# Optimization experiments

Hardware: AMD Instinct MI355X
Metric: run time of the kernel (lower is better)

## Reference

```python
import jax, jax.numpy as jnp
import numpy as np
from jax import lax

B, H, G, T = 16384, 128, 5, 12

def setup_inputs() -> dict:
    key = jax.random.key(0)
    ks = jax.random.split(key, 12)
    s = 0.05  # weight scale for numerical sanity
    return {
        "encoder_hidden": jax.random.normal(ks[0], (B, H), jnp.float32),
        "encoder_cell": jax.random.normal(ks[1], (B, H), jnp.float32),
        "last_position": jax.random.normal(ks[2], (B, 2), jnp.float32),
        "gp_w1": jax.random.normal(ks[3], (H, H), jnp.float32) * s,
        "gp_b1": jnp.zeros((H,), jnp.float32),
        "gp_w2": jax.random.normal(ks[4], (H, G * 2), jnp.float32) * s,
        "gp_b2": jnp.zeros((G * 2,), jnp.float32),
        "pr_w1": jax.random.normal(ks[5], (H, H // 2), jnp.float32) * s,
        "pr_b1": jnp.zeros((H // 2,), jnp.float32),
        "pr_w2": jax.random.normal(ks[6], (H // 2, G), jnp.float32) * s,
        "pr_b2": jnp.zeros((G,), jnp.float32),
        "w_ih": jax.random.normal(ks[7], (4, 4 * H), jnp.float32) * s,   # LSTM input weights [in=4, 4H] (i,f,g,o)
        "w_hh": jax.random.normal(ks[8], (H, 4 * H), jnp.float32) * s,   # LSTM recurrent weights [H, 4H]
        "b_ih": jnp.zeros((4 * H,), jnp.float32),
        "b_hh": jnp.zeros((4 * H,), jnp.float32),
        "ph_w": jax.random.normal(ks[9], (H, 2), jnp.float32) * s,
        "ph_b": jnp.zeros((2,), jnp.float32),
    }

def reference(encoder_hidden, encoder_cell, last_position,
              gp_w1, gp_b1, gp_w2, gp_b2,
              pr_w1, pr_b1, pr_w2, pr_b2,
              w_ih, w_hh, b_ih, b_hh, ph_w, ph_b):
    b = encoder_hidden.shape[0]
    # goal prediction: residual on last_position
    g_hid = jax.nn.relu(encoder_hidden @ gp_w1 + gp_b1)
    goals = (g_hid @ gp_w2 + gp_b2).reshape(b, G, 2) + last_position[:, None, :]  # [B,G,2]
    # goal probabilities
    p_hid = jax.nn.relu(encoder_hidden @ pr_w1 + pr_b1)
    goal_probs = jax.nn.softmax(p_hid @ pr_w2 + pr_b2, axis=-1)  # [B,G]
    # batch all goals together: leading goal dim [G,B,...]
    goals_gb = jnp.swapaxes(goals, 0, 1)                      # [G,B,2]
    h0 = jnp.broadcast_to(encoder_hidden, (G, b, H))
    c0 = jnp.broadcast_to(encoder_cell, (G, b, H))
    pos0 = jnp.broadcast_to(last_position, (G, b, 2))
    bias = b_ih + b_hh

    def step(carry, _):
        pos, h, c = carry
        x = jnp.concatenate([pos, goals_gb], axis=-1)          # [G,B,4]
        gates = x @ w_ih + h @ w_hh + bias                      # [G,B,4H]
        i, f, g, o = jnp.split(gates, 4, axis=-1)
        c_new = jax.nn.sigmoid(f) * c + jax.nn.sigmoid(i) * jnp.tanh(g)
        h_new = jax.nn.sigmoid(o) * jnp.tanh(c_new)
        pos_new = pos + (h_new @ ph_w + ph_b)                   # residual position update
        return (pos_new, h_new, c_new), pos_new

    _, path = lax.scan(step, (pos0, h0, c0), None, length=T)   # [T,G,B,2]
    predictions = jnp.transpose(path, (2, 1, 0, 3))            # [B,G,T,2]
    return predictions, goals, goal_probs
```

## Files before the change

kernel.cpp:

```cpp
#include <hip/hip_runtime.h>

#define Bn 16384
#define Hn 128
#define Gn 5
#define Tn 12

typedef __attribute__((ext_vector_type(8))) __bf16 bf16x8;
typedef __attribute__((ext_vector_type(4))) float f32x4;
typedef __attribute__((ext_vector_type(4))) unsigned int u32x4;
typedef __attribute__((ext_vector_type(2))) unsigned int u32x2;
typedef unsigned int u32;
typedef unsigned short u16;

#define MFMA(a, b, c) __builtin_amdgcn_mfma_f32_16x16x32_bf16((a), (b), (c), 0, 0, 0)

__device__ __forceinline__ u16 f2bf(float f) { return __builtin_bit_cast(u16, (__bf16)f); }
__device__ __forceinline__ u32 pk2(float a, float b) { return (u32)f2bf(a) | ((u32)f2bf(b) << 16); }

__device__ __forceinline__ int hbsw(int row, int bytein) {
    return row * 256 + ((((bytein >> 4) ^ row) & 15) << 4) + (bytein & 15);
}
__device__ __forceinline__ int pbsw(int row, int bytein) {
    return row * 128 + ((((bytein >> 4) ^ row) & 7) << 4) + (bytein & 15);
}

__global__ __launch_bounds__(256) void k_phaseA(
    const float* __restrict__ eh, const float* __restrict__ lastpos,
    const float* __restrict__ gp_w1, const float* __restrict__ gp_b1,
    const float* __restrict__ gp_w2, const float* __restrict__ gp_b2,
    const float* __restrict__ pr_w1, const float* __restrict__ pr_b1,
    const float* __restrict__ pr_w2, const float* __restrict__ pr_b2,
    float* __restrict__ goals_o, float* __restrict__ probs_o)
{
    __shared__ __align__(16) char eT[64 * 256];
    __shared__ __align__(16) char gT[64 * 256];
    __shared__ __align__(16) char pT[64 * 128];
    __shared__ float lgT[64 * 8];

    const int tid = threadIdx.x;
    const int lane = tid & 63;
    const int wv = tid >> 6;
    const int lg = lane >> 4, li = lane & 15;
    const int r0 = blockIdx.x * 64;
    const int rowbase = wv * 16;

    {
        int row = tid >> 2, seg = tid & 3;
        const float* src = eh + (size_t)(r0 + row) * Hn + seg * 32;
#pragma unroll
        for (int cc = 0; cc < 4; ++cc) {
            u32 p0 = pk2(src[cc * 8 + 0], src[cc * 8 + 1]);
            u32 p1 = pk2(src[cc * 8 + 2], src[cc * 8 + 3]);
            u32 p2 = pk2(src[cc * 8 + 4], src[cc * 8 + 5]);
            u32 p3 = pk2(src[cc * 8 + 6], src[cc * 8 + 7]);
            *(u32x4*)(eT + hbsw(row, seg * 64 + cc * 16)) = (u32x4){p0, p1, p2, p3};
        }
    }
    __syncthreads();

    bf16x8 Ae[4];
#pragma unroll
    for (int kc = 0; kc < 4; ++kc)
        Ae[kc] = *(const bf16x8*)(eT + hbsw(rowbase + li, kc * 64 + lg * 16));

#pragma unroll 1
    for (int nt = 0; nt < 8; ++nt) {
        int c1 = nt * 16 + li;
        f32x4 acc = {0.f, 0.f, 0.f, 0.f};
#pragma unroll
        for (int kc = 0; kc < 4; ++kc) {
            bf16x8 bfr;
#pragma unroll
            for (int j = 0; j < 8; ++j)
                bfr[j] = (__bf16)gp_w1[(size_t)(kc * 32 + lg * 8 + j) * Hn + c1];
            acc = MFMA(Ae[kc], bfr, acc);
        }
        float bias = gp_b1[c1];
#pragma unroll
        for (int r = 0; r < 4; ++r) {
            int row = rowbase + lg * 4 + r;
            float v = fmaxf(acc[r] + bias, 0.f);
            *(u16*)(gT + hbsw(row, c1 * 2)) = f2bf(v);
        }
    }
    __syncthreads();

    {
        bf16x8 Ag[4];
#pragma unroll
        for (int kc = 0; kc < 4; ++kc)
            Ag[kc] = *(const bf16x8*)(gT + hbsw(rowbase + li, kc * 64 + lg * 16));
        f32x4 acc = {0.f, 0.f, 0.f, 0.f};
#pragma unroll
        for (int kc = 0; kc < 4; ++kc) {
            bf16x8 bfr;
#pragma unroll
            for (int j = 0; j < 8; ++j) {
                int k = kc * 32 + lg * 8 + j;
                bfr[j] = (li < 10) ? (__bf16)gp_w2[k * 10 + li] : (__bf16)0.f;
            }
            acc = MFMA(Ag[kc], bfr, acc);
        }
        if (li < 10) {
            float b2 = gp_b2[li];
#pragma unroll
            for (int r = 0; r < 4; ++r) {
                int b = r0 + rowbase + lg * 4 + r;
                float v = acc[r] + b2 + lastpos[(size_t)b * 2 + (li & 1)];
                goals_o[(size_t)b * 10 + li] = v;
            }
        }
    }

#pragma unroll 1
    for (int nt = 0; nt < 4; ++nt) {
        int c1 = nt * 16 + li;
        f32x4 acc = {0.f, 0.f, 0.f, 0.f};
#pragma unroll
        for (int kc = 0; kc < 4; ++kc) {
            bf16x8 bfr;
#pragma unroll
            for (int j = 0; j < 8; ++j)
                bfr[j] = (__bf16)pr_w1[(size_t)(kc * 32 + lg * 8 + j) * 64 + c1];
            acc = MFMA(Ae[kc], bfr, acc);
        }
        float bias = pr_b1[c1];
#pragma unroll
        for (int r = 0; r < 4; ++r) {
            int row = rowbase + lg * 4 + r;
            float v = fmaxf(acc[r] + bias, 0.f);
            *(u16*)(pT + pbsw(row, c1 * 2)) = f2bf(v);
        }
    }
    __syncthreads();

    {
        bf16x8 Ap[2];
#pragma unroll
        for (int kc = 0; kc < 2; ++kc)
            Ap[kc] = *(const bf16x8*)(pT + pbsw(rowbase + li, kc * 64 + lg * 16));
        f32x4 acc = {0.f, 0.f, 0.f, 0.f};
#pragma unroll
        for (int kc = 0; kc < 2; ++kc) {
            bf16x8 bfr;
#pragma unroll
            for (int j = 0; j < 8; ++j) {
                int k = kc * 32 + lg * 8 + j;
                bfr[j] = (li < 5) ? (__bf16)pr_w2[k * 5 + li] : (__bf16)0.f;
            }
            acc = MFMA(Ap[kc], bfr, acc);
        }
        if (li < 5) {
            float b2 = pr_b2[li];
#pragma unroll
            for (int r = 0; r < 4; ++r) {
                int row = rowbase + lg * 4 + r;
                lgT[row * 8 + li] = acc[r] + b2;
            }
        }
    }
    __syncthreads();

    if (tid < 64) {
        int row = tid;
        float v0 = lgT[row * 8 + 0], v1 = lgT[row * 8 + 1], v2 = lgT[row * 8 + 2];
        float v3 = lgT[row * 8 + 3], v4 = lgT[row * 8 + 4];
        float mx = fmaxf(fmaxf(fmaxf(v0, v1), fmaxf(v2, v3)), v4);
        float e0 = __builtin_amdgcn_exp2f((v0 - mx) * 1.44269504f);
        float e1 = __builtin_amdgcn_exp2f((v1 - mx) * 1.44269504f);
        float e2 = __builtin_amdgcn_exp2f((v2 - mx) * 1.44269504f);
        float e3 = __builtin_amdgcn_exp2f((v3 - mx) * 1.44269504f);
        float e4 = __builtin_amdgcn_exp2f((v4 - mx) * 1.44269504f);
        float rs = __builtin_amdgcn_rcpf(e0 + e1 + e2 + e3 + e4);
        size_t ob = (size_t)(r0 + row) * 5;
        probs_o[ob + 0] = e0 * rs;
        probs_o[ob + 1] = e1 * rs;
        probs_o[ob + 2] = e2 * rs;
        probs_o[ob + 3] = e3 * rs;
        probs_o[ob + 4] = e4 * rs;
    }
}

__global__ __launch_bounds__(512) void k_lstm(
    const float* __restrict__ eh, const float* __restrict__ ec,
    const float* __restrict__ lastpos,
    const float* __restrict__ w_ih, const float* __restrict__ w_hh,
    const float* __restrict__ b_ih, const float* __restrict__ b_hh,
    const float* __restrict__ ph_w, const float* __restrict__ ph_b,
    const float* __restrict__ goals_o, float* __restrict__ preds)
{
#define MT 10
#define ROWS (MT * 16)
#define BUFB (ROWS * 256)
    __shared__ __align__(16) char hT[2][BUFB];
    __shared__ float2 posb[2][ROWS];
    __shared__ u32 gpkT[ROWS];

    const int tid = threadIdx.x;
    const int lane = tid & 63;
    const int wv = tid >> 6;
    const int lg = lane >> 4, li = lane & 15;
    const int r0 = blockIdx.x * ROWS;

    const float NL = -1.44269504f;
    const float PG = 2.88539008f;

    bf16x8 Wh[4][4];
    bf16x8 Wx[4];
#pragma unroll
    for (int gt = 0; gt < 4; ++gt) {
        const float s = (gt == 2) ? PG : NL;
        const int cg = gt * 128 + wv * 16 + li;
#pragma unroll
        for (int kc = 0; kc < 4; ++kc) {
            bf16x8 f;
#pragma unroll
            for (int j = 0; j < 8; ++j)
                f[j] = (__bf16)(w_hh[(size_t)(kc * 32 + lg * 8 + j) * 512 + cg] * s);
            Wh[gt][kc] = f;
        }
        bf16x8 fx;
#pragma unroll
        for (int j = 0; j < 8; ++j) {
            int k = lg * 8 + j;
            float v = 0.f;
            if (k < 4) v = w_ih[k * 512 + cg] * s;
            else if (k == 4) v = (b_ih[cg] + b_hh[cg]) * s;
            fx[j] = (__bf16)v;
        }
        Wx[gt] = fx;
    }

    bf16x8 php[4];
#pragma unroll
    for (int kc = 0; kc < 4; ++kc) {
        u32 w[4];
#pragma unroll
        for (int jp = 0; jp < 4; ++jp) {
            int k = kc * 32 + lg * 8 + jp * 2;
            u32 xw = pk2(ph_w[k * 2 + 0], ph_w[k * 2 + 2]);
            u32 yw = pk2(ph_w[k * 2 + 1], ph_w[k * 2 + 3]);
            w[jp] = (li == 0) ? xw : yw;
        }
        php[kc] = __builtin_bit_cast(bf16x8, (u32x4){w[0], w[1], w[2], w[3]});
    }
    const float phb0 = ph_b[0], phb1 = ph_b[1];

    const int ro0 = hbsw(li, 0 + lg * 16);
    const int ro1 = hbsw(li, 64 + lg * 16);
    const int ro2 = hbsw(li, 128 + lg * 16);
    const int ro3 = hbsw(li, 192 + lg * 16);
    const int wo  = hbsw(li, wv * 32 + lg * 8);

#pragma unroll
    for (int it = 0; it < 5; ++it) {
        int chunk = tid + it * 512;
        int row = chunk >> 4, seg = chunk & 15;
        const float* src = eh + (size_t)((r0 + row) / 5) * Hn + seg * 8;
        u32 p0 = pk2(src[0], src[1]);
        u32 p1 = pk2(src[2], src[3]);
        u32 p2 = pk2(src[4], src[5]);
        u32 p3 = pk2(src[6], src[7]);
        *(u32x4*)(hT[0] + hbsw(row, seg * 16)) = (u32x4){p0, p1, p2, p3};
    }
    if (tid < ROWS) {
        int gr = r0 + tid;
        float2 p = *(const float2*)(lastpos + (size_t)(gr / 5) * 2);
        posb[0][tid] = p;
        posb[1][tid] = p;
        float2 g2 = *(const float2*)(goals_o + (size_t)gr * 2);
        gpkT[tid] = pk2(g2.x, g2.y);
    }

    f32x4 c[MT];
#pragma unroll
    for (int m = 0; m < MT; ++m) {
        int b = (r0 + m * 16 + li) / 5;
        float4 cv = *(const float4*)(ec + (size_t)b * Hn + wv * 16 + lg * 4);
        c[m] = (f32x4){cv.x, cv.y, cv.z, cv.w};
    }

    __syncthreads();

#pragma unroll 1
    for (int t = 0; t < Tn; ++t) {
        const char* rbp = hT[0] + (t & 1) * BUFB;
        char* wbp = hT[0] + ((t & 1) ^ 1) * BUFB;
        const float2* posR = posb[t & 1];
        float2* posW = posb[(t & 1) ^ 1];
#pragma unroll
        for (int m = 0; m < MT; ++m) {
            const int mo = m * 4096;
            bf16x8 H0 = *(const bf16x8*)(rbp + ro0 + mo);
            bf16x8 H1 = *(const bf16x8*)(rbp + ro1 + mo);
            bf16x8 H2 = *(const bf16x8*)(rbp + ro2 + mo);
            bf16x8 H3 = *(const bf16x8*)(rbp + ro3 + mo);

            f32x4 a0 = {0.f, 0.f, 0.f, 0.f}, a1 = {0.f, 0.f, 0.f, 0.f};
            f32x4 a2 = {0.f, 0.f, 0.f, 0.f}, a3 = {0.f, 0.f, 0.f, 0.f};
            __builtin_amdgcn_s_setprio(1);
            a0 = MFMA(Wh[0][0], H0, a0); a1 = MFMA(Wh[1][0], H0, a1);
            a2 = MFMA(Wh[2][0], H0, a2); a3 = MFMA(Wh[3][0], H0, a3);
            a0 = MFMA(Wh[0][1], H1, a0); a1 = MFMA(Wh[1][1], H1, a1);
            a2 = MFMA(Wh[2][1], H1, a2); a3 = MFMA(Wh[3][1], H1, a3);
            a0 = MFMA(Wh[0][2], H2, a0); a1 = MFMA(Wh[1][2], H2, a1);
            a2 = MFMA(Wh[2][2], H2, a2); a3 = MFMA(Wh[3][2], H2, a3);
            a0 = MFMA(Wh[0][3], H3, a0); a1 = MFMA(Wh[1][3], H3, a1);
            a2 = MFMA(Wh[2][3], H3, a2); a3 = MFMA(Wh[3][3], H3, a3);
            __builtin_amdgcn_s_setprio(0);

            float2 pp = posR[m * 16 + li];
            float pxv = pp.x, pyv = pp.y;
            if (t > 0) {
                f32x4 pacc = {0.f, 0.f, 0.f, 0.f};
                __builtin_amdgcn_s_setprio(1);
                pacc = MFMA(php[0], H0, pacc);
                pacc = MFMA(php[1], H1, pacc);
                pacc = MFMA(php[2], H2, pacc);
                pacc = MFMA(php[3], H3, pacc);
                __builtin_amdgcn_s_setprio(0);
                pxv += pacc[0] + phb0;
                pyv += pacc[1] + phb1;
                if (((m & 7) == wv) && lg == 0) {
                    posW[m * 16 + li] = make_float2(pxv, pyv);
                    size_t o = ((size_t)(r0 + m * 16 + li) * Tn + (t - 1)) * 2;
                    *(float2*)(preds + o) = make_float2(pxv, pyv);
                }
            }

            u32 gk = gpkT[m * 16 + li];
            bf16x8 xf = __builtin_bit_cast(bf16x8,
                (u32x4){pk2(pxv, pyv), gk, 0x00003F80u, 0u});
            __builtin_amdgcn_s_setprio(1);
            a0 = MFMA(Wx[0], xf, a0);
            a1 = MFMA(Wx[1], xf, a1);
            a2 = MFMA(Wx[2], xf, a2);
            a3 = MFMA(Wx[3], xf, a3);
            __builtin_amdgcn_s_setprio(0);

            u32 w0, w1;
            {
                float hvv[4];
#pragma unroll
                for (int r = 0; r < 4; ++r) {
                    float A = __builtin_amdgcn_exp2f(a0[r]);
                    float F = __builtin_amdgcn_exp2f(a1[r]);
                    float B = __builtin_amdgcn_exp2f(a2[r]);
                    float D = __builtin_amdgcn_exp2f(a3[r]);
                    float P = (1.0f + A) * (1.0f + B);
                    float Fp = 1.0f + F;
                    float R = __builtin_amdgcn_rcpf(P * Fp);
                    float cn = (c[m][r] * P + (B - 1.0f) * Fp) * R;
                    c[m][r] = cn;
                    float C = __builtin_amdgcn_exp2f(PG * cn);
                    float R2 = __builtin_amdgcn_rcpf((1.0f + D) * (C + 1.0f));
                    hvv[r] = (C - 1.0f) * R2;
                }
                w0 = pk2(hvv[0], hvv[1]);
                w1 = pk2(hvv[2], hvv[3]);
            }
            *(u32x2*)(wbp + wo + mo) = (u32x2){w0, w1};
        }
        __syncthreads();
    }

#pragma unroll
    for (int m = 0; m < MT; ++m) {
        if ((m & 7) != wv) continue;
        const char* rbp = hT[0];
        const int mo = m * 4096;
        bf16x8 H0 = *(const bf16x8*)(rbp + ro0 + mo);
        bf16x8 H1 = *(const bf16x8*)(rbp + ro1 + mo);
        bf16x8 H2 = *(const bf16x8*)(rbp + ro2 + mo);
        bf16x8 H3 = *(const bf16x8*)(rbp + ro3 + mo);
        f32x4 pacc = {0.f, 0.f, 0.f, 0.f};
        pacc = MFMA(php[0], H0, pacc);
        pacc = MFMA(php[1], H1, pacc);
        pacc = MFMA(php[2], H2, pacc);
        pacc = MFMA(php[3], H3, pacc);
        if (lg == 0) {
            float2 pp = posb[Tn & 1][m * 16 + li];
            float fx = pp.x + pacc[0] + phb0;
            float fy = pp.y + pacc[1] + phb1;
            size_t o = ((size_t)(r0 + m * 16 + li) * Tn + (Tn - 1)) * 2;
            *(float2*)(preds + o) = make_float2(fx, fy);
        }
    }
#undef MT
#undef ROWS
#undef BUFB
}

extern "C" void kernel_launch(void* const* d_in, const int* in_sizes, int n_in,
                              void* d_out, int out_size, void* d_ws, size_t ws_size,
                              hipStream_t stream)
{
    (void)in_sizes; (void)n_in; (void)out_size; (void)d_ws; (void)ws_size;
    const float* eh   = (const float*)d_in[0];
    const float* ec   = (const float*)d_in[1];
    const float* lp   = (const float*)d_in[2];
    const float* gpw1 = (const float*)d_in[3];
    const float* gpb1 = (const float*)d_in[4];
    const float* gpw2 = (const float*)d_in[5];
    const float* gpb2 = (const float*)d_in[6];
    const float* prw1 = (const float*)d_in[7];
    const float* prb1 = (const float*)d_in[8];
    const float* prw2 = (const float*)d_in[9];
    const float* prb2 = (const float*)d_in[10];
    const float* wih  = (const float*)d_in[11];
    const float* whh  = (const float*)d_in[12];
    const float* bih  = (const float*)d_in[13];
    const float* bhh  = (const float*)d_in[14];
    const float* phw  = (const float*)d_in[15];
    const float* phb  = (const float*)d_in[16];

    float* out = (float*)d_out;
    float* preds = out;
    float* goals = out + (size_t)Bn * Gn * Tn * 2;
    float* probs = out + (size_t)Bn * Gn * Tn * 2 + (size_t)Bn * Gn * 2;

    k_phaseA<<<Bn / 64, 256, 0, stream>>>(eh, lp, gpw1, gpb1, gpw2, gpb2,
                                          prw1, prb1, prw2, prb2, goals, probs);
    k_lstm<<<(Bn * Gn) / 160, 512, 0, stream>>>(eh, ec, lp, wih, whh, bih, bhh,
                                                phw, phb, goals, preds);
}
```

Baseline: 229.2 us.

## Split LSTM gate columns across 16 waves with cross-half lane shuffle

The LSTM kernel grows from 8 to 16 waves per block. Each wave now owns 8 hidden columns instead of 16, and packs two gates into each MFMA output tile (i/f and g/o). A __shfl_xor across lane halves regathers all four gate values per element before the cell update. This halves the per-wave MFMA count and register footprint and doubles the waves available to hide latency. The cost is extra shuffles and selects, plus a heavier per-step block barrier with more waves taking part.

After: 298.0 us. 1.3x slower.

```diff
diff --git a/kernel.cpp b/kernel.cpp
--- a/kernel.cpp
+++ b/kernel.cpp
@@ -181,7 +181,7 @@
     }
 }
 
-__global__ __launch_bounds__(512) void k_lstm(
+__global__ __launch_bounds__(1024) void k_lstm(
     const float* __restrict__ eh, const float* __restrict__ ec,
     const float* __restrict__ lastpos,
     const float* __restrict__ w_ih, const float* __restrict__ w_hh,
@@ -200,24 +200,27 @@
     const int lane = tid & 63;
     const int wv = tid >> 6;
     const int lg = lane >> 4, li = lane & 15;
+    const bool lo = (lane < 32);
+    const int lgl = lg & 1;
     const int r0 = blockIdx.x * ROWS;
 
     const float NL = -1.44269504f;
     const float PG = 2.88539008f;
 
-    bf16x8 Wh[4][4];
-    bf16x8 Wx[4];
-#pragma unroll
-    for (int gt = 0; gt < 4; ++gt) {
-        const float s = (gt == 2) ? PG : NL;
-        const int cg = gt * 128 + wv * 16 + li;
+    bf16x8 Wh2[2][4];
+    bf16x8 Wx2[2];
+#pragma unroll
+    for (int grp = 0; grp < 2; ++grp) {
+        const int gate = grp * 2 + (li < 8 ? 0 : 1);
+        const int cg = gate * 128 + wv * 8 + (li & 7);
+        const float s = (gate == 2) ? PG : NL;
 #pragma unroll
         for (int kc = 0; kc < 4; ++kc) {
             bf16x8 f;
 #pragma unroll
             for (int j = 0; j < 8; ++j)
                 f[j] = (__bf16)(w_hh[(size_t)(kc * 32 + lg * 8 + j) * 512 + cg] * s);
-            Wh[gt][kc] = f;
+            Wh2[grp][kc] = f;
         }
         bf16x8 fx;
 #pragma unroll
@@ -228,7 +231,7 @@
             else if (k == 4) v = (b_ih[cg] + b_hh[cg]) * s;
             fx[j] = (__bf16)v;
         }
-        Wx[gt] = fx;
+        Wx2[grp] = fx;
     }
 
     bf16x8 php[4];
@@ -250,18 +253,17 @@
     const int ro1 = hbsw(li, 64 + lg * 16);
     const int ro2 = hbsw(li, 128 + lg * 16);
     const int ro3 = hbsw(li, 192 + lg * 16);
-    const int wo  = hbsw(li, wv * 32 + lg * 8);
+    const int hcbase = wv * 8 + lgl * 4 + (lo ? 0 : 2);
+    const int wo = hbsw(li, hcbase * 2);
 
 #pragma unroll
     for (int it = 0; it < 5; ++it) {
-        int chunk = tid + it * 512;
-        int row = chunk >> 4, seg = chunk & 15;
-        const float* src = eh + (size_t)((r0 + row) / 5) * Hn + seg * 8;
+        int chunk = tid + it * 1024;
+        int row = chunk >> 5, seg = chunk & 31;
+        const float* src = eh + (size_t)((r0 + row) / 5) * Hn + seg * 4;
         u32 p0 = pk2(src[0], src[1]);
         u32 p1 = pk2(src[2], src[3]);
-        u32 p2 = pk2(src[4], src[5]);
-        u32 p3 = pk2(src[6], src[7]);
-        *(u32x4*)(hT[0] + hbsw(row, seg * 16)) = (u32x4){p0, p1, p2, p3};
+        *(u32x2*)(hT[0] + hbsw(row, seg * 8)) = (u32x2){p0, p1};
     }
     if (tid < ROWS) {
         int gr = r0 + tid;
@@ -272,12 +274,11 @@
         gpkT[tid] = pk2(g2.x, g2.y);
     }
 
-    f32x4 c[MT];
+    float2 c[MT];
 #pragma unroll
     for (int m = 0; m < MT; ++m) {
         int b = (r0 + m * 16 + li) / 5;
-        float4 cv = *(const float4*)(ec + (size_t)b * Hn + wv * 16 + lg * 4);
-        c[m] = (f32x4){cv.x, cv.y, cv.z, cv.w};
+        c[m] = *(const float2*)(ec + (size_t)b * Hn + hcbase);
     }
 
     __syncthreads();
@@ -296,17 +297,12 @@
             bf16x8 H2 = *(const bf16x8*)(rbp + ro2 + mo);
             bf16x8 H3 = *(const bf16x8*)(rbp + ro3 + mo);
 
-            f32x4 a0 = {0.f, 0.f, 0.f, 0.f}, a1 = {0.f, 0.f, 0.f, 0.f};
-            f32x4 a2 = {0.f, 0.f, 0.f, 0.f}, a3 = {0.f, 0.f, 0.f, 0.f};
+            f32x4 aif = {0.f, 0.f, 0.f, 0.f}, ago = {0.f, 0.f, 0.f, 0.f};
             __builtin_amdgcn_s_setprio(1);
-            a0 = MFMA(Wh[0][0], H0, a0); a1 = MFMA(Wh[1][0], H0, a1);
-            a2 = MFMA(Wh[2][0], H0, a2); a3 = MFMA(Wh[3][0], H0, a3);
-            a0 = MFMA(Wh[0][1], H1, a0); a1 = MFMA(Wh[1][1], H1, a1);
-            a2 = MFMA(Wh[2][1], H1, a2); a3 = MFMA(Wh[3][1], H1, a3);
-            a0 = MFMA(Wh[0][2], H2, a0); a1 = MFMA(Wh[1][2], H2, a1);
-            a2 = MFMA(Wh[2][2], H2, a2); a3 = MFMA(Wh[3][2], H2, a3);
-            a0 = MFMA(Wh[0][3], H3, a0); a1 = MFMA(Wh[1][3], H3, a1);
-            a2 = MFMA(Wh[2][3], H3, a2); a3 = MFMA(Wh[3][3], H3, a3);
+            aif = MFMA(Wh2[0][0], H0, aif); ago = MFMA(Wh2[1][0], H0, ago);
+            aif = MFMA(Wh2[0][1], H1, aif); ago = MFMA(Wh2[1][1], H1, ago);
+            aif = MFMA(Wh2[0][2], H2, aif); ago = MFMA(Wh2[1][2], H2, ago);
+            aif = MFMA(Wh2[0][3], H3, aif); ago = MFMA(Wh2[1][3], H3, ago);
             __builtin_amdgcn_s_setprio(0);
 
             float2 pp = posR[m * 16 + li];
@@ -321,7 +317,7 @@
                 __builtin_amdgcn_s_setprio(0);
                 pxv += pacc[0] + phb0;
                 pyv += pacc[1] + phb1;
-                if (((m & 7) == wv) && lg == 0) {
+                if ((wv == m) && lg == 0) {
                     posW[m * 16 + li] = make_float2(pxv, pyv);
                     size_t o = ((size_t)(r0 + m * 16 + li) * Tn + (t - 1)) * 2;
                     *(float2*)(preds + o) = make_float2(pxv, pyv);
@@ -332,41 +328,63 @@
             bf16x8 xf = __builtin_bit_cast(bf16x8,
                 (u32x4){pk2(pxv, pyv), gk, 0x00003F80u, 0u});
             __builtin_amdgcn_s_setprio(1);
-            a0 = MFMA(Wx[0], xf, a0);
-            a1 = MFMA(Wx[1], xf, a1);
-            a2 = MFMA(Wx[2], xf, a2);
-            a3 = MFMA(Wx[3], xf, a3);
+            aif = MFMA(Wx2[0], xf, aif);
+            ago = MFMA(Wx2[1], xf, ago);
             __builtin_amdgcn_s_setprio(0);
 
-            u32 w0, w1;
+            float v_if0 = lo ? aif[2] : aif[0];
+            float v_if1 = lo ? aif[3] : aif[1];
+            float v_go0 = lo ? ago[2] : ago[0];
+            float v_go1 = lo ? ago[3] : ago[1];
+            float e_if0 = __shfl_xor(v_if0, 32);
+            float e_if1 = __shfl_xor(v_if1, 32);
+            float e_go0 = __shfl_xor(v_go0, 32);
+            float e_go1 = __shfl_xor(v_go1, 32);
+            float i0 = lo ? aif[0] : e_if0;
+            float f0 = lo ? e_if0 : aif[2];
+            float g0 = lo ? ago[0] : e_go0;
+            float o0 = lo ? e_go0 : ago[2];
+            float i1 = lo ? aif[1] : e_if1;
+            float f1 = lo ? e_if1 : aif[3];
+            float g1 = lo ? ago[1] : e_go1;
+            float o1 = lo ? e_go1 : ago[3];
+
+            float hv0, hv1;
             {
-                float hvv[4];
-#pragma unroll
-                for (int r = 0; r < 4; ++r) {
-                    float A = __builtin_amdgcn_exp2f(a0[r]);
-                    float F = __builtin_amdgcn_exp2f(a1[r]);
-                    float B = __builtin_amdgcn_exp2f(a2[r]);
-                    float D = __builtin_amdgcn_exp2f(a3[r]);
-                    float P = (1.0f + A) * (1.0f + B);
-                    float Fp = 1.0f + F;
-                    float R = __builtin_amdgcn_rcpf(P * Fp);
-                    float cn = (c[m][r] * P + (B - 1.0f) * Fp) * R;
-                    c[m][r] = cn;
-                    float C = __builtin_amdgcn_exp2f(PG * cn);
-                    float R2 = __builtin_amdgcn_rcpf((1.0f + D) * (C + 1.0f));
-                    hvv[r] = (C - 1.0f) * R2;
-                }
-                w0 = pk2(hvv[0], hvv[1]);
-                w1 = pk2(hvv[2], hvv[3]);
-            }
-            *(u32x2*)(wbp + wo + mo) = (u32x2){w0, w1};
+                float A = __builtin_amdgcn_exp2f(i0);
+                float F = __builtin_amdgcn_exp2f(f0);
+                float B = __builtin_amdgcn_exp2f(g0);
+                float D = __builtin_amdgcn_exp2f(o0);
+                float P = (1.0f + A) * (1.0f + B);
+                float Fp = 1.0f + F;
+                float R = __builtin_amdgcn_rcpf(P * Fp);
+                float cn = (c[m].x * P + (B - 1.0f) * Fp) * R;
+                c[m].x = cn;
+                float C = __builtin_amdgcn_exp2f(PG * cn);
+                float R2 = __builtin_amdgcn_rcpf((1.0f + D) * (C + 1.0f));
+                hv0 = (C - 1.0f) * R2;
+            }
+            {
+                float A = __builtin_amdgcn_exp2f(i1);
+                float F = __builtin_amdgcn_exp2f(f1);
+                float B = __builtin_amdgcn_exp2f(g1);
+                float D = __builtin_amdgcn_exp2f(o1);
+                float P = (1.0f + A) * (1.0f + B);
+                float Fp = 1.0f + F;
+                float R = __builtin_amdgcn_rcpf(P * Fp);
+                float cn = (c[m].y * P + (B - 1.0f) * Fp) * R;
+                c[m].y = cn;
+                float C = __builtin_amdgcn_exp2f(PG * cn);
+                float R2 = __builtin_amdgcn_rcpf((1.0f + D) * (C + 1.0f));
+                hv1 = (C - 1.0f) * R2;
+            }
+            *(u32*)(wbp + wo + mo) = pk2(hv0, hv1);
         }
         __syncthreads();
     }
 
-#pragma unroll
-    for (int m = 0; m < MT; ++m) {
-        if ((m & 7) != wv) continue;
+    if (wv < MT) {
+        const int m = wv;
         const char* rbp = hT[0];
         const int mo = m * 4096;
         bf16x8 H0 = *(const bf16x8*)(rbp + ro0 + mo);
@@ -421,6 +439,6 @@
 
     k_phaseA<<<Bn / 64, 256, 0, stream>>>(eh, lp, gpw1, gpb1, gpw2, gpb2,
                                           prw1, prb1, prw2, prb2, goals, probs);
-    k_lstm<<<(Bn * Gn) / 160, 512, 0, stream>>>(eh, ec, lp, wih, whh, bih, bhh,
-                                                phw, phb, goals, preds);
+    k_lstm<<<(Bn * Gn) / 160, 1024, 0, stream>>>(eh, ec, lp, wih, whh, bih, bhh,
+                                                 phw, phb, goals, preds);
 }
```
